# Optimization experiments

Measured on AMD Instinct MI355X. Metric: run time of the kernel, lower is better.

The kernel has to match this reference:

```python
import jax, jax.numpy as jnp
import numpy as np

B, N, G, K = 4, 2048, 8, 16
C_IN = K * 3 + 3  # in_features_size=0 path: conv1 in = 0 + local_n*3 + 3 = 51
CH = [C_IN, 32, 48, 64, 80, 96]  # feature_size(4i, 4i*3) = 16i for i=2..6
THR = 0.1  # weight_threshold


def setup_inputs() -> dict:
    key = jax.random.key(0)
    ks = jax.random.split(key, 3 + 3 * 5)
    inp = {
        "point_cloud": jax.random.normal(ks[0], (B, N, 3), jnp.float32),
        "normals": jax.random.normal(ks[1], (B, N, 3), jnp.float32),
        "dr_w": jax.random.uniform(ks[2], (B, N, G), jnp.float32),
    }
    for i in range(5):
        cin, cout = CH[i], CH[i + 1]
        k0 = 3 + 3 * i
        inp[f"W{i+1}"] = jax.random.normal(ks[k0], (cin, cout), jnp.float32) * (1.0 / np.sqrt(cin))
        inp[f"b{i+1}"] = jnp.zeros((cout,), jnp.float32)
        inp[f"s{i+1}"] = 1.0 + 0.1 * jax.random.normal(ks[k0 + 1], (cout,), jnp.float32)  # BN (eval) scale
        inp[f"o{i+1}"] = 0.01 * jax.random.normal(ks[k0 + 2], (cout,), jnp.float32)      # BN (eval) shift
    return inp


def _forward(point_cloud, normals, dr_w, params):
    # sign-flip group for full (non rotation-only) 3D frames: 8 ops, flips eigenvector columns
    OPS = jnp.array([[1, 1, 1], [1, 1, -1], [1, -1, 1], [1, -1, -1],
                     [-1, 1, 1], [-1, 1, -1], [-1, -1, 1], [-1, -1, -1]], jnp.float32)
    wn = jnp.swapaxes(dr_w, 1, 2)                                  # [B,G,N]
    wsum = dr_w.sum(1)                                             # [B,G]
    wnorm = dr_w / (dr_w.sum(1, keepdims=True) + 1e-6)             # [B,N,G]
    # --- get_frame (weighted): weighted center + weighted covariance + eigh per group ---
    center = jnp.einsum('bnd,bng->bgd', point_cloud, wnorm)        # [B,G,3]
    pc = point_cloud[:, None, :, :] - center[:, :, None, :]        # [B,G,N,3]
    Rm = jnp.einsum('bgnd,bgn,bgne->bgde', pc, wn, pc)             # [B,G,3,3]
    deg = (wsum > 1.0).astype(Rm.dtype)[..., None, None]           # degenerate-group guard
    noise = jax.random.normal(jax.random.key(42), Rm.shape, Rm.dtype)
    lambdas, V = jnp.linalg.eigh(deg * Rm + (1.0 - deg) * noise)
    frames = jax.lax.stop_gradient(V)                              # is_detach_frame=True
    center = jax.lax.stop_gradient(center)
    F_ops = OPS[None, :, None, None, :] * frames[:, None]          # [B,8,G,3,3]
    # --- soft-weighted kNN over points ---
    ww = jnp.einsum('bng,bmg->bnm', dr_w, dr_w)                    # [B,N,N]
    sq = jnp.sum((point_cloud[:, :, None, :] - point_cloud[:, None, :, :]) ** 2, -1)
    d = ww * sq + (1.0 - ww) * 1000.0
    _, idx = jax.lax.top_k(-d, K)                                  # smallest K -> [B,N,K]
    pnts_n = jax.vmap(lambda p, i: p[i])(point_cloud, idx)         # [B,N,K,3]
    # v1 = (1-w)*center + w*pnts_n - center = w*(pnts_n - center)
    v1 = wn[..., None, None] * (pnts_n[:, None] - center[:, :, None, None, :])  # [B,G,N,K,3]
    # v2: weighted normals blended with per-group weighted mean normal
    nw = normals[:, None, :, :] * wn[..., None]                    # [B,G,N,3]
    nmean = nw.sum(2) / (wsum[..., None] + 1e-6)                   # [B,G,3]
    v2 = nw + (1.0 - wn)[..., None] * nmean[:, :, None, :]         # [B,G,N,3]
    # apply equivariant frames: (F_ops^T @ v^T)^T == v @ F_ops
    f1 = jnp.einsum('bgnkd,bogde->bognke', v1, F_ops)              # [B,8,G,N,K,3]
    f2 = jnp.einsum('bgnd,bogde->bogne', v2, F_ops)                # [B,8,G,N,3]
    x = jnp.concatenate([f1.reshape(B, 8, G, N, K * 3), f2], -1)   # [B,8,G,N,51]
    # MinkowskiLinear + BN(eval affine) + ReLU stack, applied densely then masked
    for (W, b, s, o) in params:
        x = jax.nn.relu((x @ W + b) * s + o)
    mask = (wn >= THR).astype(x.dtype)[:, None, :, :, None]        # weight_threshold filter
    return x * mask                                                # [B,8,G,N,96]


def reference(point_cloud, normals, dr_w,
              W1, b1, s1, o1, W2, b2, s2, o2, W3, b3, s3, o3,
              W4, b4, s4, o4, W5, b5, s5, o5):
    params = [(W1, b1, s1, o1), (W2, b2, s2, o2), (W3, b3, s3, o3),
              (W4, b4, s4, o4), (W5, b5, s5, o5)]
    return _forward(point_cloud, normals, dr_w, params)
```

## Files before the change

kernel.cpp:

```cpp
#include <hip/hip_runtime.h>
#include <math.h>

#define NPTS 2048
#define BATCH 4
#define NG 8
#define KNN_K 16
#define FR_OFF 512
#define IDX_OFF 1024
#define WOFF_F (IDX_OFF + BATCH * NPTS * KNN_K)
#define FLOATMAX 3.402823466e38f

typedef __attribute__((ext_vector_type(8))) short bf16x8;
typedef __attribute__((ext_vector_type(4))) float f32x4;

__device__ inline unsigned short bf16_rne(float x) {
  unsigned u = __float_as_uint(x);
  u += 0x7FFFu + ((u >> 16) & 1u);
  return (unsigned short)(u >> 16);
}
__device__ inline float bf16_f(unsigned short h) {
  return __uint_as_float(((unsigned)h) << 16);
}

__device__ inline float slapy2f(float x, float y) {
  float ax = fabsf(x), ay = fabsf(y);
  float w = fmaxf(ax, ay), z = fminf(ax, ay);
  if (z == 0.f) return w;
  float q = z / w;
  return w * sqrtf(1.f + q * q);
}

__device__ inline void slartgf(float f, float g, float& c, float& s, float& r) {
  if (g == 0.f) { c = 1.f; s = 0.f; r = f; }
  else if (f == 0.f) { c = 0.f; s = (g >= 0.f) ? 1.f : -1.f; r = fabsf(g); }
  else {
    float d = sqrtf(f * f + g * g);
    c = fabsf(f) / d;
    r = (f >= 0.f) ? d : -d;
    s = g / r;
  }
}

__device__ void slaev2f(float a, float b, float c, float& rt1, float& rt2, float& cs1, float& sn1) {
  float sm = a + c, df = a - c, adf = fabsf(df), tb = b + b, ab = fabsf(tb);
  float acmx, acmn;
  if (fabsf(a) > fabsf(c)) { acmx = a; acmn = c; } else { acmx = c; acmn = a; }
  float rt;
  if (adf > ab) { float t = ab / adf; rt = adf * sqrtf(1.f + t * t); }
  else if (adf < ab) { float t = adf / ab; rt = ab * sqrtf(1.f + t * t); }
  else rt = ab * sqrtf(2.f);
  int sgn1;
  if (sm < 0.f) { rt1 = 0.5f * (sm - rt); sgn1 = -1; rt2 = (acmx / rt1) * acmn - (b / rt1) * b; }
  else if (sm > 0.f) { rt1 = 0.5f * (sm + rt); sgn1 = 1; rt2 = (acmx / rt1) * acmn - (b / rt1) * b; }
  else { rt1 = 0.5f * rt; rt2 = -0.5f * rt; sgn1 = 1; }
  float cs; int sgn2;
  if (df >= 0.f) { cs = df + rt; sgn2 = 1; } else { cs = df - rt; sgn2 = -1; }
  float acs = fabsf(cs);
  if (acs > ab) {
    float ct = -tb / cs;
    sn1 = 1.f / sqrtf(1.f + ct * ct);
    cs1 = ct * sn1;
  } else {
    if (ab == 0.f) { cs1 = 1.f; sn1 = 0.f; }
    else {
      float tn = -cs / tb;
      cs1 = 1.f / sqrtf(1.f + tn * tn);
      sn1 = tn * cs1;
    }
  }
  if (sgn1 == sgn2) { float tn = cs1; cs1 = -sn1; sn1 = tn; }
}

__device__ void steqr3(float d[3], float e[2], float Z[3][3]) {
  const float eps = 5.9604645e-08f;
  const float eps2 = eps * eps;
  const float safmin = 1.17549435e-38f;
  const int nmaxit = 90;
  const int n = 3;
  int jtot = 0;
  int l1 = 0;
  while (l1 <= n - 1) {
    if (l1 > 0) e[l1 - 1] = 0.f;
    int m;
    for (m = l1; m <= n - 2; m++) {
      float tst = fabsf(e[m]);
      if (tst == 0.f) break;
      if (tst <= (sqrtf(fabsf(d[m])) * sqrtf(fabsf(d[m + 1]))) * eps) { e[m] = 0.f; break; }
    }
    int l = l1, lend = m;
    l1 = m + 1;
    if (lend == l) continue;
    if (fabsf(d[lend]) < fabsf(d[l])) { int tmp = l; l = lend; lend = tmp; }
    if (lend > l) {
      for (;;) {
        int mm = lend;
        if (l != lend) {
          for (mm = l; mm <= lend - 1; mm++) {
            float tst = e[mm] * e[mm];
            if (tst <= eps2 * fabsf(d[mm]) * fabsf(d[mm + 1]) + safmin) break;
          }
        }
        if (mm < lend) e[mm] = 0.f;
        float p = d[l];
        if (mm == l) {
          d[l] = p; l++;
          if (l <= lend) continue; else break;
        }
        if (mm == l + 1) {
          float rt1, rt2, c, s;
          slaev2f(d[l], e[l], d[l + 1], rt1, rt2, c, s);
          #pragma unroll
          for (int i = 0; i < 3; i++) {
            float tp = Z[i][l + 1];
            Z[i][l + 1] = c * tp - s * Z[i][l];
            Z[i][l] = s * tp + c * Z[i][l];
          }
          d[l] = rt1; d[l + 1] = rt2; e[l] = 0.f;
          l += 2;
          if (l <= lend) continue; else break;
        }
        if (jtot == nmaxit) break;
        jtot++;
        float g = (d[l + 1] - p) / (2.f * e[l]);
        float r = slapy2f(g, 1.f);
        g = d[mm] - p + e[l] / (g + copysignf(r, g));
        float s = 1.f, c = 1.f;
        p = 0.f;
        float cs[2], sn[2];
        for (int i = mm - 1; i >= l; i--) {
          float f = s * e[i];
          float bb = c * e[i];
          slartgf(g, f, c, s, r);
          if (i != mm - 1) e[i + 1] = r;
          g = d[i + 1] - p;
          r = (d[i] - g) * s + 2.f * c * bb;
          p = s * r;
          d[i + 1] = g + p;
          g = c * r - bb;
          cs[i] = c; sn[i] = -s;
        }
        for (int jj = mm - l - 1; jj >= 0; jj--) {
          float c_ = cs[l + jj], s_ = sn[l + jj];
          #pragma unroll
          for (int i = 0; i < 3; i++) {
            float tp = Z[i][l + jj + 1];
            Z[i][l + jj + 1] = c_ * tp - s_ * Z[i][l + jj];
            Z[i][l + jj] = s_ * tp + c_ * Z[i][l + jj];
          }
        }
        d[l] -= p;
        e[l] = g;
      }
    } else {
      for (;;) {
        int mm = lend;
        if (l != lend) {
          for (mm = l; mm >= lend + 1; mm--) {
            float tst = e[mm - 1] * e[mm - 1];
            if (tst <= eps2 * fabsf(d[mm]) * fabsf(d[mm - 1]) + safmin) break;
          }
        }
        if (mm > lend) e[mm - 1] = 0.f;
        float p = d[l];
        if (mm == l) {
          d[l] = p; l--;
          if (l >= lend) continue; else break;
        }
        if (mm == l - 1) {
          float rt1, rt2, c, s;
          slaev2f(d[l - 1], e[l - 1], d[l], rt1, rt2, c, s);
          #pragma unroll
          for (int i = 0; i < 3; i++) {
            float tp = Z[i][l];
            Z[i][l] = c * tp - s * Z[i][l - 1];
            Z[i][l - 1] = s * tp + c * Z[i][l - 1];
          }
          d[l - 1] = rt1; d[l] = rt2; e[l - 1] = 0.f;
          l -= 2;
          if (l >= lend) continue; else break;
        }
        if (jtot == nmaxit) break;
        jtot++;
        float g = (d[l - 1] - p) / (2.f * e[l - 1]);
        float r = slapy2f(g, 1.f);
        g = d[mm] - p + e[l - 1] / (g + copysignf(r, g));
        float s = 1.f, c = 1.f;
        p = 0.f;
        float cs[2], sn[2];
        for (int i = mm; i <= l - 1; i++) {
          float f = s * e[i];
          float bb = c * e[i];
          slartgf(g, f, c, s, r);
          if (i != mm) e[i - 1] = r;
          g = d[i] - p;
          r = (d[i + 1] - g) * s + 2.f * c * bb;
          p = s * r;
          d[i] = g + p;
          g = c * r - bb;
          cs[i] = c; sn[i] = s;
        }
        for (int jj = 0; jj <= l - mm - 1; jj++) {
          float c_ = cs[mm + jj], s_ = sn[mm + jj];
          #pragma unroll
          for (int i = 0; i < 3; i++) {
            float tp = Z[i][mm + jj + 1];
            Z[i][mm + jj + 1] = c_ * tp - s_ * Z[i][mm + jj];
            Z[i][mm + jj] = s_ * tp + c_ * Z[i][mm + jj];
          }
        }
        d[l] -= p;
        e[l - 1] = g;
      }
    }
  }
  for (int ii = 1; ii < 3; ii++) {
    int i = ii - 1, k = i;
    float p = d[i];
    for (int j = ii; j < 3; j++) if (d[j] < p) { k = j; p = d[j]; }
    if (k != i) {
      d[k] = d[i]; d[i] = p;
      for (int r2 = 0; r2 < 3; r2++) {
        float tp = Z[r2][i]; Z[r2][i] = Z[r2][k]; Z[r2][k] = tp;
      }
    }
  }
}

__device__ void eigh_one(float* __restrict__ ws, int id) {
  const float* st = ws + id * 16;
  float A00 = st[7], A10 = st[8], A11 = st[9], A20 = st[10], A21 = st[11], A22 = st[12];

  float d[3], e[2];
  float tau = 0.f, u2 = 0.f;
  d[0] = A00;
  float alpha = A10, x31 = A20;
  if (x31 == 0.f) {
    tau = 0.f; u2 = 0.f;
    d[1] = A11; d[2] = A22; e[0] = alpha; e[1] = A21;
  } else {
    float nrm = slapy2f(alpha, fabsf(x31));
    float beta = (alpha >= 0.f) ? -nrm : nrm;
    tau = (beta - alpha) / beta;
    u2 = (1.f / (alpha - beta)) * x31;
    float x1 = tau * (A11 + A21 * u2);
    float x2 = tau * (A21 + A22 * u2);
    float al = -0.5f * tau * (x1 + x2 * u2);
    x1 = x1 + al;
    x2 = x2 + al * u2;
    d[1] = A11 - 2.f * x1;
    e[1] = A21 - (u2 * x1 + x2);
    d[2] = A22 - 2.f * (u2 * x2);
    e[0] = beta;
  }

  float Z[3][3] = {{1.f, 0.f, 0.f}, {0.f, 1.f, 0.f}, {0.f, 0.f, 1.f}};
  steqr3(d, e, Z);

  if (tau != 0.f) {
    for (int j = 0; j < 3; j++) {
      float w = Z[1][j] + u2 * Z[2][j];
      float tw = tau * w;
      Z[1][j] -= tw;
      Z[2][j] -= tw * u2;
    }
  }
  float* fr = ws + FR_OFF + id * 9;
  for (int dd = 0; dd < 3; dd++)
    for (int ee = 0; ee < 3; ee++)
      fr[dd * 3 + ee] = Z[dd][ee];
}

__global__ void prep_kernel(const float* __restrict__ pc, const float* __restrict__ nrm,
                            const float* __restrict__ drw,
                            const float* __restrict__ W1, const float* __restrict__ W2,
                            const float* __restrict__ W3, const float* __restrict__ W4,
                            const float* __restrict__ W5, float* __restrict__ ws) {
  __shared__ float red[256];
  int t = threadIdx.x;

  if (blockIdx.x < 32) {
    int bg = blockIdx.x;
    int b = bg >> 3, g = bg & 7;

    float sw = 0.f, sp0 = 0.f, sp1 = 0.f, sp2 = 0.f, sn0 = 0.f, sn1 = 0.f, sn2 = 0.f;
    for (int n = t; n < NPTS; n += 256) {
      float w = drw[((size_t)b * NPTS + n) * NG + g];
      const float* p = pc + ((size_t)b * NPTS + n) * 3;
      const float* nr = nrm + ((size_t)b * NPTS + n) * 3;
      sw += w;
      sp0 += w * p[0]; sp1 += w * p[1]; sp2 += w * p[2];
      sn0 += w * nr[0]; sn1 += w * nr[1]; sn2 += w * nr[2];
    }

    auto blockReduce = [&](float v) -> float {
      red[t] = v; __syncthreads();
      for (int s = 128; s > 0; s >>= 1) {
        if (t < s) red[t] += red[t + s];
        __syncthreads();
      }
      float r = red[0];
      __syncthreads();
      return r;
    };

    float Sw = blockReduce(sw);
    float inv = 1.f / (Sw + 1e-6f);
    float C0 = blockReduce(sp0) * inv;
    float C1 = blockReduce(sp1) * inv;
    float C2 = blockReduce(sp2) * inv;
    float M0 = blockReduce(sn0) * inv;
    float M1 = blockReduce(sn1) * inv;
    float M2 = blockReduce(sn2) * inv;

    float r00 = 0.f, r10 = 0.f, r11 = 0.f, r20 = 0.f, r21 = 0.f, r22 = 0.f;
    for (int n = t; n < NPTS; n += 256) {
      float w = drw[((size_t)b * NPTS + n) * NG + g];
      const float* p = pc + ((size_t)b * NPTS + n) * 3;
      float p0 = p[0] - C0, p1 = p[1] - C1, p2 = p[2] - C2;
      r00 += w * p0 * p0;
      r10 += w * p1 * p0;
      r11 += w * p1 * p1;
      r20 += w * p2 * p0;
      r21 += w * p2 * p1;
      r22 += w * p2 * p2;
    }
    float R00 = blockReduce(r00);
    float R10 = blockReduce(r10);
    float R11 = blockReduce(r11);
    float R20 = blockReduce(r20);
    float R21 = blockReduce(r21);
    float R22 = blockReduce(r22);

    if (t == 0) {
      float* st = ws + bg * 16;
      st[0] = Sw;
      st[1] = C0; st[2] = C1; st[3] = C2;
      st[4] = M0; st[5] = M1; st[6] = M2;
      st[7] = R00; st[8] = R10; st[9] = R11; st[10] = R20; st[11] = R21; st[12] = R22;
    }
    return;
  }

  if (t >= 64) return;
  const int FB[5] = {0, 4, 7, 15, 25};
  const int NTs[5] = {2, 3, 4, 5, 6};
  const int CINs[5] = {51, 32, 48, 64, 80};
  const int COUTs[5] = {32, 48, 64, 80, 96};
  const float* Ws[5] = {W1, W2, W3, W4, W5};

  int fp = blockIdx.x - 32;
  int layer = 0;
  while (layer < 4 && fp >= FB[layer + 1]) layer++;
  int rel = fp - FB[layer];
  int kt = rel / NTs[layer], nt = rel % NTs[layer];
  int lane = t;
  int c = nt * 16 + (lane & 15);
  int q = lane >> 4;
  int cin = CINs[layer], cout = COUTs[layer];
  const float* W = Ws[layer];

  unsigned short* wb = (unsigned short*)(ws + WOFF_F);
  unsigned short* dH = wb + fp * 1024 + lane * 8;
  unsigned short* dL = dH + 512;
  for (int i = 0; i < 8; i++) {
    int k = kt * 32 + q * 8 + i;
    float w = (k < cin) ? W[(size_t)k * cout + c] : 0.f;
    unsigned short hb = bf16_rne(w);
    dH[i] = hb;
    dL[i] = bf16_rne(w - bf16_f(hb));
  }
}

__global__ __launch_bounds__(256, 4) void knn_eigh_kernel(const float* __restrict__ pc,
                                                          const float* __restrict__ drw,
                                                          int* __restrict__ idxout,
                                                          float* __restrict__ ws) {
  if (blockIdx.x < 32) {
    if (threadIdx.x == 0) eigh_one(ws, blockIdx.x);
    return;
  }
  int t = threadIdx.x;
  int lane = t & 63;
  int q = (blockIdx.x - 32) * 4 + (t >> 6);
  int b = q >> 11;
  int n = q & (NPTS - 1);

  const float* qp = pc + ((size_t)b * NPTS + n) * 3;
  float q0 = qp[0], q1 = qp[1], q2 = qp[2];
  const float4* qw4 = (const float4*)(drw + ((size_t)b * NPTS + n) * NG);
  float4 qa = qw4[0], qb = qw4[1];

  float d[32];
  #pragma unroll
  for (int j = 0; j < 32; j++) {
    int m = j * 64 + lane;
    const float4* mw4 = (const float4*)(drw + ((size_t)b * NPTS + m) * NG);
    float4 ma = mw4[0], mb = mw4[1];
    float ww = qa.x * ma.x + qa.y * ma.y + qa.z * ma.z + qa.w * ma.w
             + qb.x * mb.x + qb.y * mb.y + qb.z * mb.z + qb.w * mb.w;
    const float* mp = pc + ((size_t)b * NPTS + m) * 3;
    float dx = q0 - mp[0], dy = q1 - mp[1], dz = q2 - mp[2];
    float sq = dx * dx + dy * dy + dz * dz;
    d[j] = ww * sq + (1.f - ww) * 1000.f;
    if ((j & 3) == 3) __builtin_amdgcn_sched_barrier(0);
  }

  int myres = 0;
  #pragma unroll 1
  for (int r = 0; r < KNN_K; r++) {
    float bd = d[0];
    int bj = 0;
    #pragma unroll
    for (int j = 1; j < 32; j++) {
      if (d[j] < bd) { bd = d[j]; bj = j; }
    }
    int gm = bj * 64 + lane;
    #pragma unroll
    for (int s = 1; s < 64; s <<= 1) {
      float od = __shfl_xor(bd, s, 64);
      int om = __shfl_xor(gm, s, 64);
      if (od < bd || (od == bd && om < gm)) { bd = od; gm = om; }
    }
    if (lane == r) myres = gm;
    int ls = gm & 63, js = gm >> 6;
    if (lane == ls) {
      #pragma unroll
      for (int j = 0; j < 32; j++) {
        if (j == js) d[j] = FLOATMAX;
      }
    }
  }
  if (lane < KNN_K) idxout[(size_t)q * KNN_K + lane] = myres;
}

#define SB0 88
#define SB1 72

template <int CIN, int COUT, int FB, int SIN, int SOUT>
__device__ inline void mfma_layer(const unsigned short* __restrict__ wfr,
                                  const unsigned short* inH, const unsigned short* inL,
                                  unsigned short* outH, unsigned short* outL,
                                  const float* __restrict__ Bb, const float* __restrict__ Ss,
                                  const float* __restrict__ Oo, int lane, int wv) {
  constexpr int KT = (CIN + 31) / 32;
  constexpr int NT = COUT / 16;
  int r = lane & 15, q = lane >> 4;
  int arow = (wv * 16 + r) * SIN;

  f32x4 acc[NT];
  #pragma unroll
  for (int i = 0; i < NT; i++) acc[i] = (f32x4){0.f, 0.f, 0.f, 0.f};

  #pragma unroll
  for (int kt = 0; kt < KT; kt++) {
    bf16x8 ah = *(const bf16x8*)(inH + arow + kt * 32 + q * 8);
    bf16x8 al = *(const bf16x8*)(inL + arow + kt * 32 + q * 8);
    #pragma unroll
    for (int nt = 0; nt < NT; nt++) {
      int fid = FB + kt * NT + nt;
      bf16x8 bh = *(const bf16x8*)(wfr + fid * 1024 + lane * 8);
      bf16x8 bl = *(const bf16x8*)(wfr + fid * 1024 + 512 + lane * 8);
      acc[nt] = __builtin_amdgcn_mfma_f32_16x16x32_bf16(ah, bh, acc[nt], 0, 0, 0);
      acc[nt] = __builtin_amdgcn_mfma_f32_16x16x32_bf16(ah, bl, acc[nt], 0, 0, 0);
      acc[nt] = __builtin_amdgcn_mfma_f32_16x16x32_bf16(al, bh, acc[nt], 0, 0, 0);
    }
  }

  #pragma unroll
  for (int nt = 0; nt < NT; nt++) {
    int c = nt * 16 + r;
    float bb = Bb[c], ss = Ss[c], oo = Oo[c];
    #pragma unroll
    for (int j = 0; j < 4; j++) {
      float h = fmaxf(fmaf(acc[nt][j] + bb, ss, oo), 0.f);
      unsigned short hb = bf16_rne(h);
      int rr = (wv * 16 + q * 4 + j) * SOUT + c;
      outH[rr] = hb;
      outL[rr] = bf16_rne(h - bf16_f(hb));
    }
  }
}

__global__ __launch_bounds__(256) void mlp_kernel(
    const float* __restrict__ pc, const float* __restrict__ nrm, const float* __restrict__ drw,
    const int* __restrict__ kidx, const float* __restrict__ ws,
    const float* __restrict__ B1, const float* __restrict__ S1, const float* __restrict__ O1,
    const float* __restrict__ B2, const float* __restrict__ S2, const float* __restrict__ O2,
    const float* __restrict__ B3, const float* __restrict__ S3, const float* __restrict__ O3,
    const float* __restrict__ B4, const float* __restrict__ S4, const float* __restrict__ O4,
    const float* __restrict__ B5, const float* __restrict__ S5, const float* __restrict__ O5,
    float* __restrict__ out) {
  __shared__ __align__(16) unsigned short smem[20480];
  unsigned short* aH0 = smem;
  unsigned short* aH1 = smem + 5632;
  unsigned short* aL0 = smem + 10240;
  unsigned short* aL1 = smem + 15872;

  int t = threadIdx.x;
  int bi = blockIdx.x;
  int b = bi >> 11;
  int g = (bi >> 8) & 7;
  int n0 = (bi & 255) << 3;
  int bg = b * 8 + g;

  {
    unsigned* z = (unsigned*)smem;
    #pragma unroll
    for (int zz = 0; zz < 40; zz++) z[zz * 256 + t] = 0u;
  }
  __syncthreads();

  if (t < 128) {
    int i = t >> 4, kk = t & 15;
    int n = n0 + i;
    int id = kidx[((size_t)b * NPTS + n) * KNN_K + kk];
    const float* p = pc + ((size_t)b * NPTS + id) * 3;
    const float* fr = ws + FR_OFF + bg * 9;
    const float* ct = ws + bg * 16 + 1;
    float w = drw[((size_t)b * NPTS + n) * NG + g];
    float v0 = w * (p[0] - ct[0]);
    float v1 = w * (p[1] - ct[1]);
    float v2 = w * (p[2] - ct[2]);
    #pragma unroll
    for (int e = 0; e < 3; e++) {
      float gv = v0 * fr[e] + v1 * fr[3 + e] + v2 * fr[6 + e];
      unsigned short hb = bf16_rne(gv);
      unsigned short lb = bf16_rne(gv - bf16_f(hb));
      int f = 3 * kk + e;
      #pragma unroll
      for (int op = 0; op < 8; op++) {
        int sb = (e == 0) ? (op >> 2) : (e == 1) ? (op >> 1) : op;
        unsigned short sgn = (unsigned short)((sb & 1) << 15);
        int rr = (i * 8 + op) * SB0 + f;
        aH0[rr] = (unsigned short)(hb ^ sgn);
        aL0[rr] = (unsigned short)(lb ^ sgn);
      }
    }
  } else if (t < 136) {
    int i = t - 128;
    int n = n0 + i;
    float w = drw[((size_t)b * NPTS + n) * NG + g];
    const float* nr = nrm + ((size_t)b * NPTS + n) * 3;
    const float* fr = ws + FR_OFF + bg * 9;
    const float* nm = ws + bg * 16 + 4;
    float v0 = nr[0] * w + (1.f - w) * nm[0];
    float v1 = nr[1] * w + (1.f - w) * nm[1];
    float v2 = nr[2] * w + (1.f - w) * nm[2];
    #pragma unroll
    for (int e = 0; e < 3; e++) {
      float gv = v0 * fr[e] + v1 * fr[3 + e] + v2 * fr[6 + e];
      unsigned short hb = bf16_rne(gv);
      unsigned short lb = bf16_rne(gv - bf16_f(hb));
      int f = 48 + e;
      #pragma unroll
      for (int op = 0; op < 8; op++) {
        int sb = (e == 0) ? (op >> 2) : (e == 1) ? (op >> 1) : op;
        unsigned short sgn = (unsigned short)((sb & 1) << 15);
        int rr = (i * 8 + op) * SB0 + f;
        aH0[rr] = (unsigned short)(hb ^ sgn);
        aL0[rr] = (unsigned short)(lb ^ sgn);
      }
    }
  }
  __syncthreads();

  const unsigned short* wfr = (const unsigned short*)(ws + WOFF_F);
  int lane = t & 63;
  int wv = t >> 6;

  mfma_layer<51, 32, 0, SB0, SB1>(wfr, aH0, aL0, aH1, aL1, B1, S1, O1, lane, wv);
  mfma_layer<32, 48, 4, SB1, SB0>(wfr, aH1, aL1, aH0, aL0, B2, S2, O2, lane, wv);
  mfma_layer<48, 64, 7, SB0, SB1>(wfr, aH0, aL0, aH1, aL1, B3, S3, O3, lane, wv);
  mfma_layer<64, 80, 15, SB1, SB0>(wfr, aH1, aL1, aH0, aL0, B4, S4, O4, lane, wv);

  {
    constexpr int KT = 3, NT = 6, FB = 25;
    int r = lane & 15, q = lane >> 4;
    int arow = (wv * 16 + r) * SB0;
    f32x4 acc[NT];
    #pragma unroll
    for (int i = 0; i < NT; i++) acc[i] = (f32x4){0.f, 0.f, 0.f, 0.f};
    #pragma unroll
    for (int kt = 0; kt < KT; kt++) {
      bf16x8 ah = *(const bf16x8*)(aH0 + arow + kt * 32 + q * 8);
      bf16x8 al = *(const bf16x8*)(aL0 + arow + kt * 32 + q * 8);
      #pragma unroll
      for (int nt = 0; nt < NT; nt++) {
        int fid = FB + kt * NT + nt;
        bf16x8 bh = *(const bf16x8*)(wfr + fid * 1024 + lane * 8);
        bf16x8 bl = *(const bf16x8*)(wfr + fid * 1024 + 512 + lane * 8);
        acc[nt] = __builtin_amdgcn_mfma_f32_16x16x32_bf16(ah, bh, acc[nt], 0, 0, 0);
        acc[nt] = __builtin_amdgcn_mfma_f32_16x16x32_bf16(ah, bl, acc[nt], 0, 0, 0);
        acc[nt] = __builtin_amdgcn_mfma_f32_16x16x32_bf16(al, bh, acc[nt], 0, 0, 0);
      }
    }
    int i = 2 * wv + (q >> 1);
    int n = n0 + i;
    float wlane = drw[((size_t)b * NPTS + n) * NG + g];
    float maskv = (wlane >= 0.1f) ? 1.f : 0.f;
    int opbase = (q & 1) * 4;
    #pragma unroll
    for (int nt = 0; nt < NT; nt++) {
      int c = nt * 16 + r;
      float bb = B5[c], ss = S5[c], oo = O5[c];
      #pragma unroll
      for (int j = 0; j < 4; j++) {
        int op = opbase + j;
        float h = fmaxf(fmaf(acc[nt][j] + bb, ss, oo), 0.f);
        out[((((size_t)(b * 8 + op)) * NG + g) * NPTS + n) * 96 + c] = h * maskv;
      }
    }
  }
}

extern "C" void kernel_launch(void* const* d_in, const int* in_sizes, int n_in,
                              void* d_out, int out_size, void* d_ws, size_t ws_size,
                              hipStream_t stream) {
  const float* pc = (const float*)d_in[0];
  const float* nrm = (const float*)d_in[1];
  const float* drw = (const float*)d_in[2];
  const float* W1 = (const float*)d_in[3];
  const float* B1 = (const float*)d_in[4];
  const float* S1 = (const float*)d_in[5];
  const float* O1 = (const float*)d_in[6];
  const float* W2 = (const float*)d_in[7];
  const float* B2 = (const float*)d_in[8];
  const float* S2 = (const float*)d_in[9];
  const float* O2 = (const float*)d_in[10];
  const float* W3 = (const float*)d_in[11];
  const float* B3 = (const float*)d_in[12];
  const float* S3 = (const float*)d_in[13];
  const float* O3 = (const float*)d_in[14];
  const float* W4 = (const float*)d_in[15];
  const float* B4 = (const float*)d_in[16];
  const float* S4 = (const float*)d_in[17];
  const float* O4 = (const float*)d_in[18];
  const float* W5 = (const float*)d_in[19];
  const float* B5 = (const float*)d_in[20];
  const float* S5 = (const float*)d_in[21];
  const float* O5 = (const float*)d_in[22];
  float* out = (float*)d_out;
  float* wsf = (float*)d_ws;
  int* idxw = (int*)(wsf + IDX_OFF);

  prep_kernel<<<75, 256, 0, stream>>>(pc, nrm, drw, W1, W2, W3, W4, W5, wsf);
  knn_eigh_kernel<<<32 + BATCH * NPTS / 4, 256, 0, stream>>>(pc, drw, idxw, wsf);
  mlp_kernel<<<BATCH * NG * (NPTS / 8), 256, 0, stream>>>(
      pc, nrm, drw, idxw, wsf,
      B1, S1, O1, B2, S2, O2, B3, S3, O3,
      B4, S4, O4, B5, S5, O5, out);
}
```

Baseline: 389.1 us.

## Pack hi/lo bf16 activations into one 32-bit LDS word per element

Activations in shared memory change from separate hi and lo bf16 arrays to one interleaved 32-bit word per element, built with a perm-based pack and split again into hi/lo vectors with perm on load. The full shared-memory zeroing pass is replaced by zeroing only the padding columns the MFMA reads, which removes one store pass. Shared memory per block shrinks and launch bounds now ask for 4 blocks per SU, aiming for higher occupancy and fewer LDS store instructions. The cost is extra perm ALU work on every activation load and possible register pressure from the occupancy hint.

```diff
diff --git a/kernel.cpp b/kernel.cpp
--- a/kernel.cpp
+++ b/kernel.cpp
@@ -20,6 +20,31 @@
 }
 __device__ inline float bf16_f(unsigned short h) {
   return __uint_as_float(((unsigned)h) << 16);
+}
+
+__device__ inline unsigned pack_hl(float h) {
+  unsigned u = __float_as_uint(h);
+  float rem = h - __uint_as_float(u & 0xffff0000u);
+  unsigned v = __float_as_uint(rem);
+  v += 0x7fffu + ((v >> 16) & 1u);
+  return __builtin_amdgcn_perm(u, v, 0x07060302u);
+}
+
+__device__ inline void unpack8(const unsigned* __restrict__ p, bf16x8& ah, bf16x8& al) {
+  union U { unsigned u[4]; bf16x8 v; };
+  uint4 x = *(const uint4*)p;
+  uint4 y = *(const uint4*)(p + 4);
+  U a, b;
+  a.u[0] = __builtin_amdgcn_perm(x.y, x.x, 0x07060302u);
+  a.u[1] = __builtin_amdgcn_perm(x.w, x.z, 0x07060302u);
+  a.u[2] = __builtin_amdgcn_perm(y.y, y.x, 0x07060302u);
+  a.u[3] = __builtin_amdgcn_perm(y.w, y.z, 0x07060302u);
+  b.u[0] = __builtin_amdgcn_perm(x.y, x.x, 0x05040100u);
+  b.u[1] = __builtin_amdgcn_perm(x.w, x.z, 0x05040100u);
+  b.u[2] = __builtin_amdgcn_perm(y.y, y.x, 0x05040100u);
+  b.u[3] = __builtin_amdgcn_perm(y.w, y.z, 0x05040100u);
+  ah = a.v;
+  al = b.v;
 }
 
 __device__ inline float slapy2f(float x, float y) {
@@ -342,7 +367,7 @@
   }
 
   if (t >= 64) return;
-  const int FB[5] = {0, 4, 7, 15, 25};
+  const int FBt[5] = {0, 4, 7, 15, 25};
   const int NTs[5] = {2, 3, 4, 5, 6};
   const int CINs[5] = {51, 32, 48, 64, 80};
   const int COUTs[5] = {32, 48, 64, 80, 96};
@@ -350,8 +375,8 @@
 
   int fp = blockIdx.x - 32;
   int layer = 0;
-  while (layer < 4 && fp >= FB[layer + 1]) layer++;
-  int rel = fp - FB[layer];
+  while (layer < 4 && fp >= FBt[layer + 1]) layer++;
+  int rel = fp - FBt[layer];
   int kt = rel / NTs[layer], nt = rel % NTs[layer];
   int lane = t;
   int c = nt * 16 + (lane & 15);
@@ -433,15 +458,14 @@
   if (lane < KNN_K) idxout[(size_t)q * KNN_K + lane] = myres;
 }
 
-#define SB0 88
-#define SB1 72
+#define PST0 84
+#define PST1 68
 
 template <int CIN, int COUT, int FB, int SIN, int SOUT>
-__device__ inline void mfma_layer(const unsigned short* __restrict__ wfr,
-                                  const unsigned short* inH, const unsigned short* inL,
-                                  unsigned short* outH, unsigned short* outL,
-                                  const float* __restrict__ Bb, const float* __restrict__ Ss,
-                                  const float* __restrict__ Oo, int lane, int wv) {
+__device__ inline void mfma_layerP(const unsigned short* __restrict__ wfr,
+                                   const unsigned* inP, unsigned* outP,
+                                   const float* __restrict__ Bb, const float* __restrict__ Ss,
+                                   const float* __restrict__ Oo, int lane, int wv) {
   constexpr int KT = (CIN + 31) / 32;
   constexpr int NT = COUT / 16;
   int r = lane & 15, q = lane >> 4;
@@ -453,8 +477,8 @@
 
   #pragma unroll
   for (int kt = 0; kt < KT; kt++) {
-    bf16x8 ah = *(const bf16x8*)(inH + arow + kt * 32 + q * 8);
-    bf16x8 al = *(const bf16x8*)(inL + arow + kt * 32 + q * 8);
+    bf16x8 ah, al;
+    unpack8(inP + arow + kt * 32 + q * 8, ah, al);
     #pragma unroll
     for (int nt = 0; nt < NT; nt++) {
       int fid = FB + kt * NT + nt;
@@ -473,15 +497,12 @@
     #pragma unroll
     for (int j = 0; j < 4; j++) {
       float h = fmaxf(fmaf(acc[nt][j] + bb, ss, oo), 0.f);
-      unsigned short hb = bf16_rne(h);
-      int rr = (wv * 16 + q * 4 + j) * SOUT + c;
-      outH[rr] = hb;
-      outL[rr] = bf16_rne(h - bf16_f(hb));
-    }
-  }
-}
-
-__global__ __launch_bounds__(256) void mlp_kernel(
+      outP[(wv * 16 + q * 4 + j) * SOUT + c] = pack_hl(h);
+    }
+  }
+}
+
+__global__ __launch_bounds__(256, 4) void mlp_kernel(
     const float* __restrict__ pc, const float* __restrict__ nrm, const float* __restrict__ drw,
     const int* __restrict__ kidx, const float* __restrict__ ws,
     const float* __restrict__ B1, const float* __restrict__ S1, const float* __restrict__ O1,
@@ -490,11 +511,9 @@
     const float* __restrict__ B4, const float* __restrict__ S4, const float* __restrict__ O4,
     const float* __restrict__ B5, const float* __restrict__ S5, const float* __restrict__ O5,
     float* __restrict__ out) {
-  __shared__ __align__(16) unsigned short smem[20480];
-  unsigned short* aH0 = smem;
-  unsigned short* aH1 = smem + 5632;
-  unsigned short* aL0 = smem + 10240;
-  unsigned short* aL1 = smem + 15872;
+  __shared__ __align__(16) unsigned smem[9728];
+  unsigned* PK0 = smem;
+  unsigned* PK1 = smem + 5376;
 
   int t = threadIdx.x;
   int bi = blockIdx.x;
@@ -503,12 +522,13 @@
   int n0 = (bi & 255) << 3;
   int bg = b * 8 + g;
 
-  {
-    unsigned* z = (unsigned*)smem;
-    #pragma unroll
-    for (int zz = 0; zz < 40; zz++) z[zz * 256 + t] = 0u;
-  }
-  __syncthreads();
+  for (int z = t; z < 1088; z += 256) {
+    int row = z / 17;
+    int cc = z - row * 17;
+    int col = (cc < 13) ? (51 + cc) : (67 + cc);
+    PK0[row * PST0 + col] = 0u;
+  }
+  if (t < 12) PK1[t] = 0u;
 
   if (t < 128) {
     int i = t >> 4, kk = t & 15;
@@ -524,16 +544,13 @@
     #pragma unroll
     for (int e = 0; e < 3; e++) {
       float gv = v0 * fr[e] + v1 * fr[3 + e] + v2 * fr[6 + e];
-      unsigned short hb = bf16_rne(gv);
-      unsigned short lb = bf16_rne(gv - bf16_f(hb));
+      unsigned pk = pack_hl(gv);
       int f = 3 * kk + e;
       #pragma unroll
       for (int op = 0; op < 8; op++) {
         int sb = (e == 0) ? (op >> 2) : (e == 1) ? (op >> 1) : op;
-        unsigned short sgn = (unsigned short)((sb & 1) << 15);
-        int rr = (i * 8 + op) * SB0 + f;
-        aH0[rr] = (unsigned short)(hb ^ sgn);
-        aL0[rr] = (unsigned short)(lb ^ sgn);
+        unsigned pv = (sb & 1) ? (pk ^ 0x80008000u) : pk;
+        PK0[(i * 8 + op) * PST0 + f] = pv;
       }
     }
   } else if (t < 136) {
@@ -549,16 +566,13 @@
     #pragma unroll
     for (int e = 0; e < 3; e++) {
       float gv = v0 * fr[e] + v1 * fr[3 + e] + v2 * fr[6 + e];
-      unsigned short hb = bf16_rne(gv);
-      unsigned short lb = bf16_rne(gv - bf16_f(hb));
+      unsigned pk = pack_hl(gv);
       int f = 48 + e;
       #pragma unroll
       for (int op = 0; op < 8; op++) {
         int sb = (e == 0) ? (op >> 2) : (e == 1) ? (op >> 1) : op;
-        unsigned short sgn = (unsigned short)((sb & 1) << 15);
-        int rr = (i * 8 + op) * SB0 + f;
-        aH0[rr] = (unsigned short)(hb ^ sgn);
-        aL0[rr] = (unsigned short)(lb ^ sgn);
+        unsigned pv = (sb & 1) ? (pk ^ 0x80008000u) : pk;
+        PK0[(i * 8 + op) * PST0 + f] = pv;
       }
     }
   }
@@ -568,22 +582,22 @@
   int lane = t & 63;
   int wv = t >> 6;
 
-  mfma_layer<51, 32, 0, SB0, SB1>(wfr, aH0, aL0, aH1, aL1, B1, S1, O1, lane, wv);
-  mfma_layer<32, 48, 4, SB1, SB0>(wfr, aH1, aL1, aH0, aL0, B2, S2, O2, lane, wv);
-  mfma_layer<48, 64, 7, SB0, SB1>(wfr, aH0, aL0, aH1, aL1, B3, S3, O3, lane, wv);
-  mfma_layer<64, 80, 15, SB1, SB0>(wfr, aH1, aL1, aH0, aL0, B4, S4, O4, lane, wv);
+  mfma_layerP<51, 32, 0, PST0, PST1>(wfr, PK0, PK1, B1, S1, O1, lane, wv);
+  mfma_layerP<32, 48, 4, PST1, PST0>(wfr, PK1, PK0, B2, S2, O2, lane, wv);
+  mfma_layerP<48, 64, 7, PST0, PST1>(wfr, PK0, PK1, B3, S3, O3, lane, wv);
+  mfma_layerP<64, 80, 15, PST1, PST0>(wfr, PK1, PK0, B4, S4, O4, lane, wv);
 
   {
     constexpr int KT = 3, NT = 6, FB = 25;
     int r = lane & 15, q = lane >> 4;
-    int arow = (wv * 16 + r) * SB0;
+    int arow = (wv * 16 + r) * PST0;
     f32x4 acc[NT];
     #pragma unroll
     for (int i = 0; i < NT; i++) acc[i] = (f32x4){0.f, 0.f, 0.f, 0.f};
     #pragma unroll
     for (int kt = 0; kt < KT; kt++) {
-      bf16x8 ah = *(const bf16x8*)(aH0 + arow + kt * 32 + q * 8);
-      bf16x8 al = *(const bf16x8*)(aL0 + arow + kt * 32 + q * 8);
+      bf16x8 ah, al;
+      unpack8(PK0 + arow + kt * 32 + q * 8, ah, al);
       #pragma unroll
       for (int nt = 0; nt < NT; nt++) {
         int fid = FB + kt * NT + nt;
```

New measurement: 388.2 us. About the same (-0.2%).
